# Performance work log

Measured on AMD Instinct MI355X. Metric: run time of the kernel, lower is better.

Reference implementation:

```python
import jax, jax.numpy as jnp
import numpy as np

D_K = 128


def setup_inputs() -> dict:
    key = jax.random.key(0)
    k = jax.random.split(key, 5)
    B, H, H_KV, S_Q, S_PAST, D = 2, 16, 4, 1024, 1024, D_K
    return {
        "Q": jax.random.normal(k[0], (B, H, S_Q, D), dtype=jnp.float32),
        "K": jax.random.normal(k[1], (B, H, S_Q, D), dtype=jnp.float32),
        "V": jax.random.normal(k[2], (B, H, S_Q, D), dtype=jnp.float32),
        "past_key": jax.random.normal(k[3], (B, H_KV, S_PAST, D), dtype=jnp.float32),
        "past_value": jax.random.normal(k[4], (B, H_KV, S_PAST, D), dtype=jnp.float32),
    }


def reference(Q, K, V, past_key, past_value):
    B, H, S_q, D = Q.shape
    H_kv = past_key.shape[1]
    n_groups = H // H_kv
    scale = 1.0 / jnp.sqrt(jnp.float32(D_K))

    # expand_grouped_kv: [B,H_kv,S,D] -> [B,H_kv,G,S,D] -> [B,H,S,D] == repeat along heads
    pk = jnp.repeat(past_key, n_groups, axis=1)
    pv = jnp.repeat(past_value, n_groups, axis=1)
    K_full = jnp.concatenate([pk, K], axis=2)   # [B,H,S_k,D]
    V_full = jnp.concatenate([pv, V], axis=2)
    present_key = K_full[:, ::n_groups]         # [B,H_kv,S_present,D]
    present_value = V_full[:, ::n_groups]

    S_k = K_full.shape[2]
    scores = jnp.einsum("bhqd,bhkd->bhqk", Q, K_full) * scale  # [B,H,S_q,S_k]
    start = S_k - S_q
    # torch.tril(ones(S_q,S_k), diagonal=start): key j visible iff j <= q + start
    causal = jnp.arange(S_k)[None, :] <= (jnp.arange(S_q)[:, None] + start)
    scores = jnp.where(causal[None, None], scores, jnp.float32(-jnp.inf))
    attn = jax.nn.softmax(scores, axis=-1)
    out = jnp.einsum("bhqk,bhkd->bhqd", attn, V_full)
    return out, present_key, present_value
```

## Files before the change

### kernel.cpp

```cpp
#include <hip/hip_runtime.h>
#include <hip/hip_bf16.h>

#define B_    2
#define H_    16
#define HKV_  4
#define SQ_   1024
#define SP_   1024
#define SK_   2048
#define D_    128
#define QBLK  64
#define KVBLK 64

typedef __attribute__((ext_vector_type(8))) __bf16 bf16x8;
typedef __attribute__((ext_vector_type(4))) __bf16 bf16x4;
typedef __attribute__((ext_vector_type(4))) float  f32x4;

__device__ inline __bf16 f2bf(float f) { return (__bf16)f; }

__global__ __launch_bounds__(256, 2)
void attn_fused_kernel(const float* __restrict__ Q, const float* __restrict__ Kin,
                       const float* __restrict__ Vin, const float* __restrict__ PK,
                       const float* __restrict__ PV, float* __restrict__ Out,
                       float* __restrict__ opk, float* __restrict__ opv)
{
    __shared__ __align__(16) __bf16 Klds[KVBLK * D_];
    __shared__ __align__(16) __bf16 Vlds[D_ * KVBLK];
    __shared__ __align__(16) __bf16 Plds[4 * 16 * KVBLK];

    const int tid = threadIdx.x;
    const int id  = blockIdx.x;

    if (id >= 512) {
        const int cid = id - 512;
        const int bgc = cid & 7;
        const int sub = cid >> 3;
        const int isV = sub >> 2;
        const int q4  = sub & 3;
        const int bb = bgc >> 2, g = bgc & 3;
        const float* past = isV ? PV : PK;
        const float* cur  = isV ? Vin : Kin;
        float* dst = isV ? opv : opk;
        const int base = bgc*65536 + q4*16384;
        #pragma unroll 4
        for (int i = 0; i < 64; ++i) {
            int id2 = base + i*256 + tid;
            int d4 = id2 & 31;
            int s  = (id2 >> 5) & (SK_-1);
            const float* srcp = (s < SP_)
                ? past + (((size_t)bgc)*SP_ + s)*(size_t)D_ + d4*4
                : cur  + (((size_t)(bb*H_ + 4*g))*SQ_ + (s - SP_))*(size_t)D_ + d4*4;
            float4 v = *(const float4*)srcp;
            *(float4*)(dst + (size_t)id2*4) = v;
        }
        return;
    }

    const int grp = id & 7;
    const int rest = id >> 3;
    const int hi  = rest & 3;
    const int qt  = rest >> 2;
    const int b   = grp >> 2;
    const int h   = (grp & 3)*4 + hi;

    const int lane = tid & 63;
    const int w    = tid >> 6;
    const int lr   = lane & 15;
    const int lg   = lane >> 4;
    const int q0w  = qt * QBLK + w * 16;

    const float scale_l2e = 0.08838834764831845f * 1.4426950408889634f;

    bf16x8 qf[4];
    {
        const float* qsrc = Q + (((size_t)b*H_ + h)*SQ_ + q0w + lr)*(size_t)D_ + lg*8;
        #pragma unroll
        for (int c = 0; c < 4; ++c) {
            f32x4 a0 = *(const f32x4*)(qsrc + c*32);
            f32x4 a1 = *(const f32x4*)(qsrc + c*32 + 4);
            bf16x8 f;
            #pragma unroll
            for (int j = 0; j < 4; ++j) {
                f[j]   = f2bf(a0[j] * scale_l2e);
                f[j+4] = f2bf(a1[j] * scale_l2e);
            }
            qf[c] = f;
        }
    }

    f32x4 o[8];
    #pragma unroll
    for (int i = 0; i < 8; ++i) o[i] = (f32x4){0.f,0.f,0.f,0.f};
    float m_r = -1e30f, l_r = 0.f;

    const int nt = qt + 17;
    const size_t pk_base = (((size_t)b*HKV_ + (h>>2))*SP_)*(size_t)D_;
    const size_t kn_base = (((size_t)b*H_   + h     )*SQ_)*(size_t)D_;

    f32x4 kreg[4][2], vreg[2][4];

    auto loadKV = [&](const float* ks, const float* vs) {
        #pragma unroll
        for (int i = 0; i < 4; ++i) {
            int idx = i*256 + tid, row = idx >> 4, c8 = idx & 15;
            kreg[i][0] = *(const f32x4*)(ks + row*D_ + c8*8);
            kreg[i][1] = *(const f32x4*)(ks + row*D_ + c8*8 + 4);
        }
        #pragma unroll
        for (int i = 0; i < 2; ++i) {
            int blk = i*256 + tid, bk = blk & 15, bd = blk >> 4;
            #pragma unroll
            for (int kk = 0; kk < 4; ++kk)
                vreg[i][kk] = *(const f32x4*)(vs + (4*bk+kk)*D_ + bd*4);
        }
    };

    loadKV(PK + pk_base, PV + pk_base);

    for (int kt = 0; kt < nt; ++kt) {
        const int k0 = kt * KVBLK;
        __syncthreads();

        #pragma unroll
        for (int i = 0; i < 4; ++i) {
            int idx = i*256 + tid, row = idx >> 4, c8 = idx & 15;
            bf16x8 f;
            #pragma unroll
            for (int j = 0; j < 4; ++j) {
                f[j]   = f2bf(kreg[i][0][j]);
                f[j+4] = f2bf(kreg[i][1][j]);
            }
            int off = (row*256 + c8*16) ^ ((row & 7) << 4);
            *(bf16x8*)((char*)Klds + off) = f;
        }
        #pragma unroll
        for (int i = 0; i < 2; ++i) {
            int blk = i*256 + tid, bk = blk & 15, bd = blk >> 4;
            #pragma unroll
            for (int j = 0; j < 4; ++j) {
                int d = 4*bd + j;
                bf16x4 t;
                t[0]=f2bf(vreg[i][0][j]); t[1]=f2bf(vreg[i][1][j]);
                t[2]=f2bf(vreg[i][2][j]); t[3]=f2bf(vreg[i][3][j]);
                int off = (d*128 + bk*8) ^ ((d & 7) << 4);
                *(bf16x4*)((char*)Vlds + off) = t;
            }
        }
        __syncthreads();

        if (kt + 1 < nt) {
            const int k1 = k0 + KVBLK;
            const float* ks = (k1 < SP_) ? PK + pk_base + (size_t)k1*D_
                                         : Kin + kn_base + (size_t)(k1 - SP_)*D_;
            const float* vs = (k1 < SP_) ? PV + pk_base + (size_t)k1*D_
                                         : Vin + kn_base + (size_t)(k1 - SP_)*D_;
            loadKV(ks, vs);
        }

        f32x4 s[4];
        #pragma unroll
        for (int n = 0; n < 4; ++n) s[n] = (f32x4){0.f,0.f,0.f,0.f};
        #pragma unroll
        for (int n = 0; n < 4; ++n) {
            #pragma unroll
            for (int c = 0; c < 4; ++c) {
                int off = ((n*16 + lr)*256 + c*64 + lg*16) ^ ((lr & 7) << 4);
                bf16x8 kf = *(const bf16x8*)((char*)Klds + off);
                s[n] = __builtin_amdgcn_mfma_f32_16x16x32_bf16(kf, qf[c], s[n], 0, 0, 0);
            }
        }

        float p[16];
        const bool needmask = (k0 + KVBLK - 1) > (q0w + SP_);
        if (needmask) {
            const int qv = q0w + lr + SP_;
            #pragma unroll
            for (int n = 0; n < 4; ++n)
                #pragma unroll
                for (int r = 0; r < 4; ++r) {
                    int kg = k0 + n*16 + lg*4 + r;
                    p[n*4+r] = (kg <= qv) ? s[n][r] : -1e30f;
                }
        } else {
            #pragma unroll
            for (int n = 0; n < 4; ++n)
                #pragma unroll
                for (int r = 0; r < 4; ++r) p[n*4+r] = s[n][r];
        }

        float mx = p[0];
        #pragma unroll
        for (int i = 1; i < 16; ++i) mx = fmaxf(mx, p[i]);
        mx = fmaxf(mx, __shfl_xor(mx, 16));
        mx = fmaxf(mx, __shfl_xor(mx, 32));
        if (!__all(mx <= m_r + 8.0f)) {
            float mnew  = fmaxf(m_r, mx);
            float alpha = exp2f(m_r - mnew);
            m_r = mnew;
            l_r *= alpha;
            #pragma unroll
            for (int dt = 0; dt < 8; ++dt) {
                o[dt][0] *= alpha; o[dt][1] *= alpha;
                o[dt][2] *= alpha; o[dt][3] *= alpha;
            }
        }
        float psum = 0.f;
        #pragma unroll
        for (int i = 0; i < 16; ++i) { p[i] = exp2f(p[i] - m_r); psum += p[i]; }
        psum += __shfl_xor(psum, 16);
        psum += __shfl_xor(psum, 32);
        l_r += psum;

        char* Pw = (char*)Plds + w*2048;
        #pragma unroll
        for (int n = 0; n < 4; ++n) {
            bf16x4 t;
            t[0]=f2bf(p[n*4+0]); t[1]=f2bf(p[n*4+1]);
            t[2]=f2bf(p[n*4+2]); t[3]=f2bf(p[n*4+3]);
            int off = (lr*128 + n*32 + lg*8) ^ ((lr & 7) << 4);
            *(bf16x4*)(Pw + off) = t;
        }

        #pragma unroll
        for (int kk = 0; kk < 2; ++kk) {
            int poff = (lr*128 + kk*64 + lg*16) ^ ((lr & 7) << 4);
            bf16x8 pa = *(const bf16x8*)(Pw + poff);
            #pragma unroll
            for (int dt = 0; dt < 8; ++dt) {
                int voff = ((dt*16 + lr)*128 + kk*64 + lg*16) ^ ((lr & 7) << 4);
                bf16x8 vf = *(const bf16x8*)((char*)Vlds + voff);
                o[dt] = __builtin_amdgcn_mfma_f32_16x16x32_bf16(vf, pa, o[dt], 0, 0, 0);
            }
        }
    }

    float inv = 1.0f / l_r;
    float* orow = Out + (((size_t)b*H_ + h)*SQ_ + q0w + lr)*(size_t)D_;
    #pragma unroll
    for (int dt = 0; dt < 8; ++dt) {
        f32x4 st;
        st[0]=o[dt][0]*inv; st[1]=o[dt][1]*inv;
        st[2]=o[dt][2]*inv; st[3]=o[dt][3]*inv;
        *(f32x4*)(orow + dt*16 + lg*4) = st;
    }
}

extern "C" void kernel_launch(void* const* d_in, const int* in_sizes, int n_in,
                              void* d_out, int out_size, void* d_ws, size_t ws_size,
                              hipStream_t stream) {
    const float* Q   = (const float*)d_in[0];
    const float* K   = (const float*)d_in[1];
    const float* V   = (const float*)d_in[2];
    const float* PK  = (const float*)d_in[3];
    const float* PV  = (const float*)d_in[4];
    float* out = (float*)d_out;
    float* opk = out + (size_t)B_*H_*SQ_*D_;
    float* opv = opk + (size_t)B_*HKV_*SK_*D_;

    attn_fused_kernel<<<576, 256, 0, stream>>>(Q, K, V, PK, PV, out, opk, opv);
}
```

Before: 81.21 us.

## Pre-convert K/V tiles to swizzled bf16 workspace and stream them via async LDS loads

Adds a prep kernel that converts each 64-row K/V tile to bf16 in the swizzled, transposed LDS layout once. It stores these tiles in the workspace and also writes the present_key/value copies. The attention kernel then double-buffers tiles straight into LDS with global_load_lds, which removes the repeated fp32 loads and per-block conversion (past KV was converted four times, once per group head). The cost is an extra kernel launch, a workspace round trip, and a fallback path used when the workspace is too small.

```diff
diff --git a/kernel.cpp b/kernel.cpp
--- a/kernel.cpp
+++ b/kernel.cpp
@@ -10,6 +10,9 @@
 #define D_    128
 #define QBLK  64
 #define KVBLK 64
+#define TILEB 32768
+#define NPAST 128
+#define NTILES 640
 
 typedef __attribute__((ext_vector_type(8))) __bf16 bf16x8;
 typedef __attribute__((ext_vector_type(4))) __bf16 bf16x4;
@@ -17,11 +20,273 @@
 
 __device__ inline __bf16 f2bf(float f) { return (__bf16)f; }
 
+__device__ inline void gl_lds16(const char* g, char* l) {
+    __builtin_amdgcn_global_load_lds(
+        (const __attribute__((address_space(1))) void*)g,
+        (__attribute__((address_space(3))) void*)l, 16, 0, 0);
+}
+
+__global__ __launch_bounds__(256)
+void prep_kernel(const float* __restrict__ Kin, const float* __restrict__ Vin,
+                 const float* __restrict__ PK,  const float* __restrict__ PV,
+                 float* __restrict__ opk, float* __restrict__ opv, char* __restrict__ ws)
+{
+    __shared__ __align__(16) char Tl[TILEB];
+    const int tid = threadIdx.x;
+    const int id  = blockIdx.x;
+
+    const float *ksrc, *vsrc;
+    float *pkdst = nullptr, *pvdst = nullptr;
+    size_t tidx;
+    if (id < NPAST) {
+        int grp = id & 7, kt = id >> 3;
+        int s0 = kt * 64;
+        ksrc = PK + (((size_t)grp)*SP_ + s0)*(size_t)D_;
+        vsrc = PV + (((size_t)grp)*SP_ + s0)*(size_t)D_;
+        pkdst = opk + (((size_t)grp)*SK_ + s0)*(size_t)D_;
+        pvdst = opv + (((size_t)grp)*SK_ + s0)*(size_t)D_;
+        tidx = (size_t)(grp*16 + kt);
+    } else {
+        int nid = id - NPAST;
+        int h16 = nid >> 4;
+        int ktp = nid & 15;
+        int bb = h16 >> 4, hh = h16 & 15;
+        int s0 = ktp * 64;
+        ksrc = Kin + (((size_t)h16)*SQ_ + s0)*(size_t)D_;
+        vsrc = Vin + (((size_t)h16)*SQ_ + s0)*(size_t)D_;
+        if ((hh & 3) == 0) {
+            int grp = bb*4 + (hh >> 2);
+            pkdst = opk + (((size_t)grp)*SK_ + SP_ + s0)*(size_t)D_;
+            pvdst = opv + (((size_t)grp)*SK_ + SP_ + s0)*(size_t)D_;
+        }
+        tidx = (size_t)(NPAST + nid);
+    }
+
+    #pragma unroll
+    for (int i = 0; i < 4; ++i) {
+        int idx = i*256 + tid, row = idx >> 4, c8 = idx & 15;
+        f32x4 a0 = *(const f32x4*)(ksrc + row*D_ + c8*8);
+        f32x4 a1 = *(const f32x4*)(ksrc + row*D_ + c8*8 + 4);
+        if (pkdst) {
+            *(f32x4*)(pkdst + row*D_ + c8*8)     = a0;
+            *(f32x4*)(pkdst + row*D_ + c8*8 + 4) = a1;
+        }
+        bf16x8 f;
+        #pragma unroll
+        for (int j = 0; j < 4; ++j) { f[j] = f2bf(a0[j]); f[j+4] = f2bf(a1[j]); }
+        int off = (row*256 + c8*16) ^ ((row & 7) << 4);
+        *(bf16x8*)(Tl + off) = f;
+    }
+    #pragma unroll
+    for (int i = 0; i < 2; ++i) {
+        int blk = i*256 + tid, bk = blk & 15, bd = blk >> 4;
+        f32x4 vr[4];
+        #pragma unroll
+        for (int kk = 0; kk < 4; ++kk)
+            vr[kk] = *(const f32x4*)(vsrc + (4*bk+kk)*D_ + bd*4);
+        #pragma unroll
+        for (int j = 0; j < 4; ++j) {
+            int d = 4*bd + j;
+            bf16x4 t;
+            t[0]=f2bf(vr[0][j]); t[1]=f2bf(vr[1][j]);
+            t[2]=f2bf(vr[2][j]); t[3]=f2bf(vr[3][j]);
+            int off = (d*128 + bk*8) ^ ((d & 7) << 4);
+            *(bf16x4*)(Tl + 16384 + off) = t;
+        }
+    }
+    if (pvdst) {
+        #pragma unroll
+        for (int i = 0; i < 4; ++i) {
+            int idx = i*256 + tid, row = idx >> 4, c8 = idx & 15;
+            *(f32x4*)(pvdst + row*D_ + c8*8)     = *(const f32x4*)(vsrc + row*D_ + c8*8);
+            *(f32x4*)(pvdst + row*D_ + c8*8 + 4) = *(const f32x4*)(vsrc + row*D_ + c8*8 + 4);
+        }
+    }
+    __syncthreads();
+    char* dst = ws + tidx*TILEB;
+    #pragma unroll
+    for (int i = 0; i < 8; ++i) {
+        int off = i*4096 + tid*16;
+        *(f32x4*)(dst + off) = *(const f32x4*)(Tl + off);
+    }
+}
+
 __global__ __launch_bounds__(256, 2)
-void attn_fused_kernel(const float* __restrict__ Q, const float* __restrict__ Kin,
-                       const float* __restrict__ Vin, const float* __restrict__ PK,
-                       const float* __restrict__ PV, float* __restrict__ Out,
-                       float* __restrict__ opk, float* __restrict__ opv)
+void attn_lean_kernel(const float* __restrict__ Q, float* __restrict__ Out,
+                      const char* __restrict__ ws)
+{
+    __shared__ __align__(16) char Kb2[2][16384];
+    __shared__ __align__(16) char Vb2[2][16384];
+    __shared__ __align__(16) char Pl[8192];
+
+    const int tid = threadIdx.x;
+    const int id  = blockIdx.x;
+    const int grp  = id & 7;
+    const int rest = id >> 3;
+    const int hi   = rest & 3;
+    const int qt   = rest >> 2;
+    const int b    = grp >> 2;
+    const int h    = (grp & 3)*4 + hi;
+    const int h16  = b*16 + h;
+
+    const int lane = tid & 63;
+    const int w    = tid >> 6;
+    const int lr   = lane & 15;
+    const int lg   = lane >> 4;
+    const int q0w  = qt * QBLK + w * 16;
+    const int nt   = qt + 17;
+
+    const float scale_l2e = 0.08838834764831845f * 1.4426950408889634f;
+
+    const char* tiles = ws;
+    const int boff = w*1024 + lane*16;
+    auto STAGE = [&](int buf, int kt) {
+        size_t t = (kt < 16) ? (size_t)(grp*16 + kt) : (size_t)(NPAST + h16*16 + (kt - 16));
+        const char* src = tiles + t*TILEB;
+        char* kb = Kb2[buf];
+        char* vb = Vb2[buf];
+        #pragma unroll
+        for (int i = 0; i < 4; ++i) gl_lds16(src + i*4096 + boff,         kb + i*4096 + w*1024);
+        #pragma unroll
+        for (int i = 0; i < 4; ++i) gl_lds16(src + 16384 + i*4096 + boff, vb + i*4096 + w*1024);
+    };
+
+    STAGE(0, 0);
+
+    bf16x8 qf[4];
+    {
+        const float* qsrc = Q + (((size_t)h16)*SQ_ + q0w + lr)*(size_t)D_ + lg*8;
+        #pragma unroll
+        for (int c = 0; c < 4; ++c) {
+            f32x4 a0 = *(const f32x4*)(qsrc + c*32);
+            f32x4 a1 = *(const f32x4*)(qsrc + c*32 + 4);
+            bf16x8 f;
+            #pragma unroll
+            for (int j = 0; j < 4; ++j) {
+                f[j]   = f2bf(a0[j] * scale_l2e);
+                f[j+4] = f2bf(a1[j] * scale_l2e);
+            }
+            qf[c] = f;
+        }
+    }
+
+    f32x4 o[8];
+    #pragma unroll
+    for (int i = 0; i < 8; ++i) o[i] = (f32x4){0.f,0.f,0.f,0.f};
+    float m_r = -1e30f, l_r = 0.f;
+
+    for (int kt = 0; kt < nt; ++kt) {
+        const int cur = kt & 1;
+        if (kt + 1 < nt) {
+            STAGE(cur ^ 1, kt + 1);
+            asm volatile("s_waitcnt vmcnt(8)" ::: "memory");
+        } else {
+            asm volatile("s_waitcnt vmcnt(0)" ::: "memory");
+        }
+        __builtin_amdgcn_sched_barrier(0);
+        __builtin_amdgcn_s_barrier();
+        __builtin_amdgcn_sched_barrier(0);
+
+        const char* Kbp = Kb2[cur];
+        const char* Vbp = Vb2[cur];
+
+        f32x4 s[4];
+        #pragma unroll
+        for (int n = 0; n < 4; ++n) s[n] = (f32x4){0.f,0.f,0.f,0.f};
+        #pragma unroll
+        for (int n = 0; n < 4; ++n) {
+            #pragma unroll
+            for (int c = 0; c < 4; ++c) {
+                int off = ((n*16 + lr)*256 + c*64 + lg*16) ^ ((lr & 7) << 4);
+                bf16x8 kf = *(const bf16x8*)(Kbp + off);
+                s[n] = __builtin_amdgcn_mfma_f32_16x16x32_bf16(kf, qf[c], s[n], 0, 0, 0);
+            }
+        }
+
+        const int k0 = kt * KVBLK;
+        float p[16];
+        const bool needmask = (k0 + KVBLK - 1) > (q0w + SP_);
+        if (needmask) {
+            const int qv = q0w + lr + SP_;
+            #pragma unroll
+            for (int n = 0; n < 4; ++n)
+                #pragma unroll
+                for (int r = 0; r < 4; ++r) {
+                    int kg = k0 + n*16 + lg*4 + r;
+                    p[n*4+r] = (kg <= qv) ? s[n][r] : -1e30f;
+                }
+        } else {
+            #pragma unroll
+            for (int n = 0; n < 4; ++n)
+                #pragma unroll
+                for (int r = 0; r < 4; ++r) p[n*4+r] = s[n][r];
+        }
+
+        float mx = p[0];
+        #pragma unroll
+        for (int i = 1; i < 16; ++i) mx = fmaxf(mx, p[i]);
+        mx = fmaxf(mx, __shfl_xor(mx, 16));
+        mx = fmaxf(mx, __shfl_xor(mx, 32));
+        if (!__all(mx <= m_r + 8.0f)) {
+            float mnew  = fmaxf(m_r, mx);
+            float alpha = exp2f(m_r - mnew);
+            m_r = mnew;
+            l_r *= alpha;
+            #pragma unroll
+            for (int dt = 0; dt < 8; ++dt) {
+                o[dt][0] *= alpha; o[dt][1] *= alpha;
+                o[dt][2] *= alpha; o[dt][3] *= alpha;
+            }
+        }
+        float psum = 0.f;
+        #pragma unroll
+        for (int i = 0; i < 16; ++i) { p[i] = exp2f(p[i] - m_r); psum += p[i]; }
+        psum += __shfl_xor(psum, 16);
+        psum += __shfl_xor(psum, 32);
+        l_r += psum;
+
+        char* Pw = Pl + w*2048;
+        #pragma unroll
+        for (int n = 0; n < 4; ++n) {
+            bf16x4 t;
+            t[0]=f2bf(p[n*4+0]); t[1]=f2bf(p[n*4+1]);
+            t[2]=f2bf(p[n*4+2]); t[3]=f2bf(p[n*4+3]);
+            int off = (lr*128 + n*32 + lg*8) ^ ((lr & 7) << 4);
+            *(bf16x4*)(Pw + off) = t;
+        }
+
+        #pragma unroll
+        for (int kk = 0; kk < 2; ++kk) {
+            int poff = (lr*128 + kk*64 + lg*16) ^ ((lr & 7) << 4);
+            bf16x8 pa = *(const bf16x8*)(Pw + poff);
+            #pragma unroll
+            for (int dt = 0; dt < 8; ++dt) {
+                int voff = ((dt*16 + lr)*128 + kk*64 + lg*16) ^ ((lr & 7) << 4);
+                bf16x8 vf = *(const bf16x8*)(Vbp + voff);
+                o[dt] = __builtin_amdgcn_mfma_f32_16x16x32_bf16(vf, pa, o[dt], 0, 0, 0);
+            }
+        }
+
+        __builtin_amdgcn_sched_barrier(0);
+        __builtin_amdgcn_s_barrier();
+    }
+
+    float inv = 1.0f / l_r;
+    float* orow = Out + (((size_t)h16)*SQ_ + q0w + lr)*(size_t)D_;
+    #pragma unroll
+    for (int dt = 0; dt < 8; ++dt) {
+        f32x4 st;
+        st[0]=o[dt][0]*inv; st[1]=o[dt][1]*inv;
+        st[2]=o[dt][2]*inv; st[3]=o[dt][3]*inv;
+        *(f32x4*)(orow + dt*16 + lg*4) = st;
+    }
+}
+
+__global__ __launch_bounds__(256, 2)
+void attn_fallback_kernel(const float* __restrict__ Q, const float* __restrict__ Kin,
+                          const float* __restrict__ Vin, const float* __restrict__ PK,
+                          const float* __restrict__ PV, float* __restrict__ Out,
+                          float* __restrict__ opk, float* __restrict__ opv)
 {
     __shared__ __align__(16) __bf16 Klds[KVBLK * D_];
     __shared__ __align__(16) __bf16 Vlds[D_ * KVBLK];
@@ -55,12 +320,12 @@
         return;
     }
 
-    const int grp = id & 7;
+    const int grp  = id & 7;
     const int rest = id >> 3;
-    const int hi  = rest & 3;
-    const int qt  = rest >> 2;
-    const int b   = grp >> 2;
-    const int h   = (grp & 3)*4 + hi;
+    const int hi   = rest & 3;
+    const int qt   = rest >> 2;
+    const int b    = grp >> 2;
+    const int h    = (grp & 3)*4 + hi;
 
     const int lane = tid & 63;
     const int w    = tid >> 6;
@@ -97,7 +362,6 @@
     const size_t kn_base = (((size_t)b*H_   + h     )*SQ_)*(size_t)D_;
 
     f32x4 kreg[4][2], vreg[2][4];
-
     auto loadKV = [&](const float* ks, const float* vs) {
         #pragma unroll
         for (int i = 0; i < 4; ++i) {
@@ -119,7 +383,6 @@
     for (int kt = 0; kt < nt; ++kt) {
         const int k0 = kt * KVBLK;
         __syncthreads();
-
         #pragma unroll
         for (int i = 0; i < 4; ++i) {
             int idx = i*256 + tid, row = idx >> 4, c8 = idx & 15;
@@ -256,5 +519,12 @@
     float* opk = out + (size_t)B_*H_*SQ_*D_;
     float* opv = opk + (size_t)B_*HKV_*SK_*D_;
 
-    attn_fused_kernel<<<576, 256, 0, stream>>>(Q, K, V, PK, PV, out, opk, opv);
+    const size_t NEED = (size_t)NTILES * TILEB;
+    if (ws_size >= NEED) {
+        char* ws = (char*)d_ws;
+        prep_kernel<<<NTILES, 256, 0, stream>>>(K, V, PK, PV, opk, opv, ws);
+        attn_lean_kernel<<<512, 256, 0, stream>>>(Q, out, ws);
+    } else {
+        attn_fallback_kernel<<<576, 256, 0, stream>>>(Q, K, V, PK, PV, out, opk, opv);
+    }
 }
```

New measurement: 82.76 us. About the same (+1.9%).
